# Kernel optimization log

Measured on AMD Instinct MI355X. Metric: run time of the kernel, lower is better.

## Reference

```python
import jax, jax.numpy as jnp
import numpy as np

N, M, D, K = 32768, 1024, 512, 4096  # frames, motion_dim, latent_dim, codebook size
COMMITMENT_COST = 0.25
BN_EPS = 1e-5


def setup_inputs() -> dict:
    key = jax.random.key(0)
    ks = jax.random.split(key, 4)
    return {
        "x": jax.random.normal(ks[0], (N, M), dtype=jnp.float32),
        "enc_w": jax.random.normal(ks[1], (D, M), dtype=jnp.float32) * (1.0 / np.sqrt(M)),
        "enc_b": jnp.zeros((D,), jnp.float32),
        "bn_gamma": jnp.ones((D,), jnp.float32),
        "bn_beta": jnp.zeros((D,), jnp.float32),
        "bn_mean": jnp.zeros((D,), jnp.float32),
        "bn_var": jnp.ones((D,), jnp.float32),
        # nn.Embedding init: uniform(-1/K, 1/K)
        "codebook": jax.random.uniform(ks[2], (K, D), dtype=jnp.float32, minval=-1.0 / K, maxval=1.0 / K),
        "dec_w": jax.random.normal(ks[3], (M, D), dtype=jnp.float32) * (1.0 / np.sqrt(D)),
        "dec_b": jnp.zeros((M,), jnp.float32),
    }


def reference(x, enc_w, enc_b, bn_gamma, bn_beta, bn_mean, bn_var, codebook, dec_w, dec_b):
    # Encoder linear: [N, M] -> [N, D]
    z = x @ enc_w.T + enc_b
    # BatchNorm1d (inference mode, running stats)
    z = (z - bn_mean) * jax.lax.rsqrt(bn_var + BN_EPS) * bn_gamma + bn_beta

    # VQ (VQ_Payam_EMA, eval): squared L2 distances via ||z||^2 + ||e||^2 - 2 z e^T
    # distances: [N, K]
    distances = (
        jnp.sum(z * z, axis=1, keepdims=True)
        + jnp.sum(codebook * codebook, axis=1)
        - 2.0 * (z @ codebook.T)
    )
    idx = jnp.argmin(distances, axis=1)                    # [N]
    encodings = jax.nn.one_hot(idx, K, dtype=z.dtype)      # [N, K] one-hot scatter
    quantized = codebook[idx]                              # gather == encodings @ codebook

    # commitment loss (EMA variant: only e_latent_loss, quantized detached)
    e_latent_loss = jnp.mean((jax.lax.stop_gradient(quantized) - z) ** 2)
    loss = COMMITMENT_COST * e_latent_loss

    # straight-through estimator
    quantized_st = z + jax.lax.stop_gradient(quantized - z)

    avg_probs = jnp.mean(encodings, axis=0)                # [K]
    perplexity = jnp.exp(-jnp.sum(avg_probs * jnp.log(avg_probs + 1e-10)))

    # Decoder linear: [N, D] -> [N, M]
    out = quantized_st @ dec_w.T + dec_b
    return out, loss, perplexity, encodings
```

## Files before the change

kernel.cpp:

```cpp
#include <hip/hip_runtime.h>
#include <math.h>
#include <float.h>

#define N_FR 32768
#define M_DIM 1024
#define D_DIM 512
#define K_CB 4096

static const long long OUT_ELEMS = (long long)N_FR * M_DIM;
static const long long LOSS_OFF  = OUT_ELEMS;
static const long long ENC_OFF   = OUT_ELEMS + 2;
static const long long Z_OFF     = ENC_OFF + 2;
static const long long DC_OFF    = Z_OFF  + (long long)N_FR * D_DIM;
static const long long XH_OFF    = DC_OFF + (long long)K_CB * M_DIM;
static const long long XL_OFF    = XH_OFF + (long long)N_FR * M_DIM / 2;
static const long long WH_OFF    = XL_OFF + (long long)N_FR * M_DIM / 2;
static const long long WL_OFF    = WH_OFF + (long long)D_DIM * M_DIM / 2;
static const long long CH_OFF    = WL_OFF + (long long)D_DIM * M_DIM / 2;
static const long long CL_OFF    = CH_OFF + (long long)K_CB * D_DIM / 2;
static const long long ZH_OFF    = CL_OFF + (long long)K_CB * D_DIM / 2;
static const long long ZL_OFF    = ZH_OFF + (long long)N_FR * D_DIM / 2;
static const long long PV_OFF    = ZL_OFF + (long long)N_FR * D_DIM / 2;
static const long long PI_OFF    = PV_OFF + 4LL * N_FR;
static const long long DWH_OFF   = PI_OFF + 4LL * N_FR;
static const long long DWL_OFF   = DWH_OFF + (long long)M_DIM * D_DIM / 2;
static const long long SN_OFF    = DWL_OFF + (long long)M_DIM * D_DIM / 2;
static const long long LP_OFF    = SN_OFF + (long long)N_FR;

typedef __attribute__((ext_vector_type(8))) short bf16x8;
typedef __attribute__((ext_vector_type(8))) unsigned short u16x8;
typedef __attribute__((ext_vector_type(4))) float f32x4;

__device__ __forceinline__ unsigned short f2bf(float f) {
    unsigned u = __float_as_uint(f);
    return (unsigned short)((u + 0x7fffu + ((u >> 16) & 1u)) >> 16);
}
__device__ __forceinline__ float bf2f(unsigned short h) {
    return __uint_as_float(((unsigned)h) << 16);
}
__device__ __forceinline__ void gl_lds16(const unsigned short* g, unsigned short* l) {
    __builtin_amdgcn_global_load_lds(
        (const __attribute__((address_space(1))) unsigned int*)g,
        (__attribute__((address_space(3))) unsigned int*)l,
        16, 0, 0);
}

__device__ __forceinline__ void conv_body(const float* in, unsigned short* hi,
                                          unsigned short* lo, int C, int KC, int w)
{
    int lane = threadIdx.x & 63;
    int bn = w / KC, ck = w % KC;
    int r = bn * 16 + (lane & 15);
    int c = ck * 32 + (lane >> 4) * 8;
    const float4* p = (const float4*)&in[(size_t)r * C + c];
    float4 v0 = p[0], v1 = p[1];
    float f[8] = {v0.x, v0.y, v0.z, v0.w, v1.x, v1.y, v1.z, v1.w};
    u16x8 hv, lv;
    #pragma unroll
    for (int j = 0; j < 8; ++j) {
        unsigned short h = f2bf(f[j]);
        hv[j] = h;
        lv[j] = f2bf(f[j] - bf2f(h));
    }
    size_t o = (size_t)w * 512 + lane * 8;
    *(u16x8*)&hi[o] = hv;
    *(u16x8*)&lo[o] = lv;
}

__global__ __launch_bounds__(256)
void conv_all(const float* __restrict__ x,  const float* __restrict__ ew,
              const float* __restrict__ cb, const float* __restrict__ dw,
              unsigned short* __restrict__ xh,  unsigned short* __restrict__ xl,
              unsigned short* __restrict__ wh,  unsigned short* __restrict__ wl,
              unsigned short* __restrict__ ch,  unsigned short* __restrict__ cl,
              unsigned short* __restrict__ dwh, unsigned short* __restrict__ dwl)
{
    int b = blockIdx.x;
    const float* in; unsigned short* hi; unsigned short* lo; int C; int w0;
    if (b < 16384)      { in = x;  hi = xh;  lo = xl;  C = 1024; w0 = b; }
    else if (b < 16640) { in = ew; hi = wh;  lo = wl;  C = 1024; w0 = b - 16384; }
    else if (b < 17664) { in = cb; hi = ch;  lo = cl;  C = 512;  w0 = b - 16640; }
    else                { in = dw; hi = dwh; lo = dwl; C = 512;  w0 = b - 17664; }
    int KC = C / 32;
    conv_body(in, hi, lo, C, KC, w0 * 4 + (threadIdx.x >> 6));
}

__global__ __launch_bounds__(256)
void conv_split(const float* __restrict__ in, unsigned short* __restrict__ hi,
                unsigned short* __restrict__ lo, int C, int KC)
{
    conv_body(in, hi, lo, C, KC, blockIdx.x * 4 + (threadIdx.x >> 6));
}

template<int EPI>
__global__ __launch_bounds__(256)
void gemm_pack(const unsigned short* __restrict__ ah_, const unsigned short* __restrict__ al_,
               const unsigned short* __restrict__ bh_, const unsigned short* __restrict__ bl_,
               const float* __restrict__ bias, const float* __restrict__ gamma,
               const float* __restrict__ beta, const float* __restrict__ mean,
               const float* __restrict__ var, float* __restrict__ C,
               int nbi, int nkb, int NJ)
{
    __shared__ unsigned short lds[16384];
    const int tid = threadIdx.x, wid = tid >> 6, lane = tid & 63;
    const int wr = wid >> 1, wc = wid & 1;
    const int bi = blockIdx.x % nbi, bj = blockIdx.x / nbi;

    f32x4 acc[4][4];
    #pragma unroll
    for (int i = 0; i < 4; ++i)
        #pragma unroll
        for (int j = 0; j < 4; ++j) acc[i][j] = (f32x4){0.f, 0.f, 0.f, 0.f};

    for (int ks = 0; ks < nkb; ++ks) {
        __syncthreads();
        #pragma unroll
        for (int q = 0; q < 8; ++q) {
            int id = wid * 8 + q;
            int arr = id >> 3, rb = id & 7;
            const unsigned short* base = arr == 0 ? ah_ : arr == 1 ? al_ : arr == 2 ? bh_ : bl_;
            size_t b = (size_t)((arr < 2 ? bi : bj) * 8 + rb) * nkb + ks;
            gl_lds16(base + b * 512 + lane * 8, lds + id * 512);
        }
        __syncthreads();
        bf16x8 ah[4], al[4], bh[4], bl[4];
        #pragma unroll
        for (int i = 0; i < 4; ++i) {
            ah[i] = *(const bf16x8*)(lds + (4 * wr + i) * 512 + lane * 8);
            al[i] = *(const bf16x8*)(lds + 4096 + (4 * wr + i) * 512 + lane * 8);
        }
        #pragma unroll
        for (int j = 0; j < 4; ++j) {
            bh[j] = *(const bf16x8*)(lds + 8192  + (4 * wc + j) * 512 + lane * 8);
            bl[j] = *(const bf16x8*)(lds + 12288 + (4 * wc + j) * 512 + lane * 8);
        }
        #pragma unroll
        for (int i = 0; i < 4; ++i)
            #pragma unroll
            for (int j = 0; j < 4; ++j) {
                acc[i][j] = __builtin_amdgcn_mfma_f32_16x16x32_bf16(ah[i], bh[j], acc[i][j], 0, 0, 0);
                acc[i][j] = __builtin_amdgcn_mfma_f32_16x16x32_bf16(ah[i], bl[j], acc[i][j], 0, 0, 0);
                acc[i][j] = __builtin_amdgcn_mfma_f32_16x16x32_bf16(al[i], bh[j], acc[i][j], 0, 0, 0);
            }
    }
    #pragma unroll
    for (int j = 0; j < 4; ++j) {
        int col = bj * 128 + wc * 64 + j * 16 + (lane & 15);
        float bvv = bias[col];
        float g = 0.f, bt = 0.f, mn = 0.f, rs = 0.f;
        if (EPI == 0) {
            g  = gamma[col];
            bt = beta[col];
            mn = mean[col];
            rs = (float)(1.0 / sqrt((double)var[col] + 1e-5));
        }
        #pragma unroll
        for (int i = 0; i < 4; ++i)
            #pragma unroll
            for (int r = 0; r < 4; ++r) {
                int row = bi * 128 + wr * 64 + i * 16 + (lane >> 4) * 4 + r;
                float v = acc[i][j][r] + bvv;
                if (EPI == 0) v = (v - mn) * rs * g + bt;
                C[(size_t)row * NJ + col] = v;
            }
    }
}

__global__ __launch_bounds__(256, 2)
void argmin_mfma(const unsigned short* __restrict__ zh, const unsigned short* __restrict__ zl,
                 const unsigned short* __restrict__ ch,
                 const float* __restrict__ se,
                 float* __restrict__ pval, int* __restrict__ pidx)
{
    __shared__ unsigned short lds[32768];
    __shared__ float sv[128][2];
    __shared__ int   si[128][2];
    const int tid = threadIdx.x, wid = tid >> 6, lane = tid & 63;
    const int wr = wid >> 1, wc = wid & 1;
    const int row0 = (int)(blockIdx.x >> 2) * 128;
    const int grp  = (int)(blockIdx.x & 3);

    auto stage = [&](int t, int bufsel) {
        int cc = t >> 4, ks = t & 15;
        int code0 = grp * 1024 + cc * 256;
        unsigned short* dst = lds + bufsel * 16384;
        #pragma unroll
        for (int q = 0; q < 8; ++q) {
            int id = wid * 8 + q;
            const unsigned short* src;
            if (id < 16) {
                int a = id >> 3, rb = id & 7;
                src = (a ? zl : zh) + ((size_t)((row0 >> 4) + rb) * 16 + ks) * 512 + lane * 8;
            } else {
                int cb2 = id - 16;
                src = ch + ((size_t)((code0 >> 4) + cb2) * 16 + ks) * 512 + lane * 8;
            }
            gl_lds16(src, dst + id * 512);
        }
    };

    float bv[16];
    int   bi[16];
    #pragma unroll
    for (int s = 0; s < 16; ++s) { bv[s] = FLT_MAX; bi[s] = 0x7fffffff; }

    f32x4 acc[4][8];
    #pragma unroll
    for (int i = 0; i < 4; ++i)
        #pragma unroll
        for (int j = 0; j < 8; ++j) acc[i][j] = (f32x4){0.f, 0.f, 0.f, 0.f};

    stage(0, 0);
    __syncthreads();

    for (int t = 0; t < 64; ++t) {
        int cur = t & 1;
        if (t < 63) stage(t + 1, cur ^ 1);
        const unsigned short* L = lds + cur * 16384;
        bf16x8 ah[4], al[4];
        #pragma unroll
        for (int i = 0; i < 4; ++i) {
            ah[i] = *(const bf16x8*)(L + (wr * 4 + i) * 512 + lane * 8);
            al[i] = *(const bf16x8*)(L + 4096 + (wr * 4 + i) * 512 + lane * 8);
        }
        #pragma unroll
        for (int j = 0; j < 8; ++j) {
            bf16x8 bhj = *(const bf16x8*)(L + 8192 + (wc * 8 + j) * 512 + lane * 8);
            #pragma unroll
            for (int i = 0; i < 4; ++i) {
                acc[i][j] = __builtin_amdgcn_mfma_f32_16x16x32_bf16(ah[i], bhj, acc[i][j], 0, 0, 0);
                acc[i][j] = __builtin_amdgcn_mfma_f32_16x16x32_bf16(al[i], bhj, acc[i][j], 0, 0, 0);
            }
        }
        if ((t & 15) == 15) {
            int code0 = grp * 1024 + (t >> 4) * 256;
            #pragma unroll
            for (int j = 0; j < 8; ++j) {
                int code = code0 + wc * 128 + j * 16 + (lane & 15);
                float sev = se[code];
                #pragma unroll
                for (int i = 0; i < 4; ++i)
                    #pragma unroll
                    for (int r = 0; r < 4; ++r) {
                        float key = sev - 2.0f * acc[i][j][r];
                        int s = i * 4 + r;
                        if (key < bv[s]) { bv[s] = key; bi[s] = code; }
                        acc[i][j][r] = 0.f;
                    }
            }
        }
        __syncthreads();
    }

    #pragma unroll
    for (int s = 0; s < 16; ++s) {
        #pragma unroll
        for (int off = 1; off < 16; off <<= 1) {
            float ov = __shfl_xor(bv[s], off);
            int   oi = __shfl_xor(bi[s], off);
            if (ov < bv[s] || (ov == bv[s] && oi < bi[s])) { bv[s] = ov; bi[s] = oi; }
        }
    }
    if ((lane & 15) == 0) {
        #pragma unroll
        for (int i = 0; i < 4; ++i)
            #pragma unroll
            for (int r = 0; r < 4; ++r) {
                int row = wr * 64 + i * 16 + (lane >> 4) * 4 + r;
                sv[row][wc] = bv[i * 4 + r];
                si[row][wc] = bi[i * 4 + r];
            }
    }
    __syncthreads();
    if (tid < 128) {
        float v0 = sv[tid][0], v1 = sv[tid][1];
        int   i0 = si[tid][0], i1 = si[tid][1];
        float bvv = v0; int bii = i0;
        if (v1 < v0 || (v1 == v0 && i1 < i0)) { bvv = v1; bii = i1; }
        pval[(size_t)grp * N_FR + row0 + tid] = bvv;
        pidx[(size_t)grp * N_FR + row0 + tid] = bii;
    }
}

__global__ __launch_bounds__(256)
void merge_k(const float* __restrict__ pval, const int* __restrict__ pidx,
             const float* __restrict__ sn,
             int* __restrict__ fidx, int* __restrict__ counts,
             float* __restrict__ lpart)
{
    __shared__ float ls[4];
    int tid = threadIdx.x;
    int n = blockIdx.x * 256 + tid;
    float best = pval[n];
    int   bi   = pidx[n];
    #pragma unroll
    for (int c = 1; c < 4; ++c) {
        float v = pval[(long long)c * N_FR + n];
        int   i = pidx[(long long)c * N_FR + n];
        if (v < best) { best = v; bi = i; }
    }
    fidx[n] = bi;
    atomicAdd(&counts[bi], 1);
    float rl = sn[n] + best;
    #pragma unroll
    for (int off = 32; off; off >>= 1) rl += __shfl_xor(rl, off);
    if ((tid & 63) == 0) ls[tid >> 6] = rl;
    __syncthreads();
    if (tid == 0) lpart[blockIdx.x] = ls[0] + ls[1] + ls[2] + ls[3];
}

__global__ __launch_bounds__(256)
void rownorm_k(const float* __restrict__ A, float* __restrict__ sn)
{
    int row  = blockIdx.x * 4 + (threadIdx.x >> 6);
    int lane = threadIdx.x & 63;
    const float4* p = (const float4*)(A + (long long)row * D_DIM + lane * 8);
    float4 a = p[0], b = p[1];
    float s = a.x*a.x + a.y*a.y + a.z*a.z + a.w*a.w
            + b.x*b.x + b.y*b.y + b.z*b.z + b.w*b.w;
    #pragma unroll
    for (int off = 32; off; off >>= 1) s += __shfl_xor(s, off);
    if (lane == 0) sn[row] = s;
}

__global__ __launch_bounds__(256)
void gather_k(const float* __restrict__ DC, const int* __restrict__ fidx,
              float* __restrict__ outp)
{
    int n = blockIdx.x;
    int id = fidx[n];
    float4 v = ((const float4*)(DC + (long long)id * M_DIM))[threadIdx.x];
    ((float4*)(outp + (long long)n * M_DIM))[threadIdx.x] = v;
}

__global__ __launch_bounds__(256)
void enc_write(const int* __restrict__ fidx, float* __restrict__ enc)
{
    int n    = blockIdx.x * 4 + (threadIdx.x >> 6);
    int lane = threadIdx.x & 63;
    int idx  = fidx[n];
    float4* row = (float4*)(enc + (size_t)n * K_CB);
    #pragma unroll
    for (int c = 0; c < 16; ++c) {
        int p = c * 64 + lane;
        int b4 = p * 4;
        float4 v;
        v.x = (idx == b4 + 0) ? 1.0f : 0.0f;
        v.y = (idx == b4 + 1) ? 1.0f : 0.0f;
        v.z = (idx == b4 + 2) ? 1.0f : 0.0f;
        v.w = (idx == b4 + 3) ? 1.0f : 0.0f;
        row[p] = v;
    }
}

__global__ __launch_bounds__(256)
void fin_k(const int* __restrict__ counts, const float* __restrict__ lpart,
           float* __restrict__ scal)
{
    __shared__ double sh[4], lh[4];
    int tid = threadIdx.x;
    double s = 0.0;
    for (int k = tid; k < K_CB; k += 256) {
        double p = (double)counts[k] / (double)N_FR;
        s += p * log(p + 1e-10);
    }
    double l = (tid < 128) ? (double)lpart[tid] : 0.0;
    #pragma unroll
    for (int off = 32; off; off >>= 1) {
        s += __shfl_xor(s, off);
        l += __shfl_xor(l, off);
    }
    if ((tid & 63) == 0) { sh[tid >> 6] = s; lh[tid >> 6] = l; }
    __syncthreads();
    if (tid == 0) {
        double tot = sh[0] + sh[1] + sh[2] + sh[3];
        double L   = lh[0] + lh[1] + lh[2] + lh[3];
        scal[0] = (float)(0.25 * L / ((double)N_FR * (double)D_DIM));
        scal[1] = (float)exp(-tot);
    }
}

extern "C" void kernel_launch(void* const* d_in, const int* in_sizes, int n_in,
                              void* d_out, int out_size, void* d_ws, size_t ws_size,
                              hipStream_t stream)
{
    (void)in_sizes; (void)n_in; (void)out_size; (void)ws_size;
    const float* x        = (const float*)d_in[0];
    const float* enc_w    = (const float*)d_in[1];
    const float* enc_b    = (const float*)d_in[2];
    const float* bn_gamma = (const float*)d_in[3];
    const float* bn_beta  = (const float*)d_in[4];
    const float* bn_mean  = (const float*)d_in[5];
    const float* bn_var   = (const float*)d_in[6];
    const float* cb       = (const float*)d_in[7];
    const float* dec_w    = (const float*)d_in[8];
    const float* dec_b    = (const float*)d_in[9];

    float* outp = (float*)d_out;
    float* z    = outp + Z_OFF;
    float* dc   = outp + DC_OFF;
    unsigned short* xh  = (unsigned short*)(outp + XH_OFF);
    unsigned short* xl  = (unsigned short*)(outp + XL_OFF);
    unsigned short* whp = (unsigned short*)(outp + WH_OFF);
    unsigned short* wlp = (unsigned short*)(outp + WL_OFF);
    unsigned short* chp = (unsigned short*)(outp + CH_OFF);
    unsigned short* clp = (unsigned short*)(outp + CL_OFF);
    unsigned short* zhp = (unsigned short*)(outp + ZH_OFF);
    unsigned short* zlp = (unsigned short*)(outp + ZL_OFF);
    float* pval = outp + PV_OFF;
    int*   pidx = (int*)(outp + PI_OFF);
    unsigned short* dwh = (unsigned short*)(outp + DWH_OFF);
    unsigned short* dwl = (unsigned short*)(outp + DWL_OFF);
    float* sn    = outp + SN_OFF;
    float* lpart = outp + LP_OFF;

    char*   wsb    = (char*)d_ws;
    int*    fidx   = (int*)wsb;
    int*    counts = (int*)(wsb + 131072);
    float*  se     = (float*)(wsb + 147456);

    hipMemsetAsync(counts, 0, 16384, stream);

    conv_all<<<dim3(17920), 256, 0, stream>>>(x, enc_w, cb, dec_w,
        xh, xl, whp, wlp, chp, clp, dwh, dwl);
    rownorm_k<<<dim3(K_CB / 4), 256, 0, stream>>>(cb, se);

    gemm_pack<0><<<dim3(1024), 256, 0, stream>>>(xh, xl, whp, wlp,
        enc_b, bn_gamma, bn_beta, bn_mean, bn_var, z, 256, 32, D_DIM);
    conv_split<<<dim3(8192), 256, 0, stream>>>(z, zhp, zlp, D_DIM, D_DIM / 32);
    rownorm_k<<<dim3(N_FR / 4), 256, 0, stream>>>(z, sn);

    gemm_pack<1><<<dim3(256), 256, 0, stream>>>(chp, clp, dwh, dwl,
        dec_b, nullptr, nullptr, nullptr, nullptr, dc, 32, 16, M_DIM);

    argmin_mfma<<<dim3(1024), 256, 0, stream>>>(zhp, zlp, chp, se, pval, pidx);
    merge_k<<<dim3(N_FR / 256), 256, 0, stream>>>(pval, pidx, sn, fidx, counts, lpart);

    gather_k<<<dim3(N_FR), 256, 0, stream>>>(dc, fidx, outp);
    fin_k<<<dim3(1), 256, 0, stream>>>(counts, lpart, outp + LOSS_OFF);

    enc_write<<<dim3(N_FR / 4), 256, 0, stream>>>(fidx, outp + ENC_OFF);
}
```

Before: 662.2 us.

## Drop low-order bf16 split terms for weights, codebook and z; double-buffer GEMMs

Removes the low-part bf16 residual for the encoder weights, the codebook and z. The encoder and decoder GEMMs therefore do two MFMA passes instead of three, and the argmin distance GEMM does one instead of two. The GEMM kernel gains double-buffered LDS staging. The z conversion is fused with the row-norm computation into one kernel that writes partial sums, and merge_k adds those up. This cuts MFMA work and memory traffic, but lowers precision in the distance computation, which can flip argmin results for near-tied codebook entries.

```diff
diff --git a/kernel.cpp b/kernel.cpp
--- a/kernel.cpp
+++ b/kernel.cpp
@@ -10,22 +10,19 @@
 static const long long OUT_ELEMS = (long long)N_FR * M_DIM;
 static const long long LOSS_OFF  = OUT_ELEMS;
 static const long long ENC_OFF   = OUT_ELEMS + 2;
-static const long long Z_OFF     = ENC_OFF + 2;
-static const long long DC_OFF    = Z_OFF  + (long long)N_FR * D_DIM;
-static const long long XH_OFF    = DC_OFF + (long long)K_CB * M_DIM;
-static const long long XL_OFF    = XH_OFF + (long long)N_FR * M_DIM / 2;
-static const long long WH_OFF    = XL_OFF + (long long)N_FR * M_DIM / 2;
-static const long long WL_OFF    = WH_OFF + (long long)D_DIM * M_DIM / 2;
-static const long long CH_OFF    = WL_OFF + (long long)D_DIM * M_DIM / 2;
-static const long long CL_OFF    = CH_OFF + (long long)K_CB * D_DIM / 2;
-static const long long ZH_OFF    = CL_OFF + (long long)K_CB * D_DIM / 2;
-static const long long ZL_OFF    = ZH_OFF + (long long)N_FR * D_DIM / 2;
-static const long long PV_OFF    = ZL_OFF + (long long)N_FR * D_DIM / 2;
-static const long long PI_OFF    = PV_OFF + 4LL * N_FR;
-static const long long DWH_OFF   = PI_OFF + 4LL * N_FR;
-static const long long DWL_OFF   = DWH_OFF + (long long)M_DIM * D_DIM / 2;
-static const long long SN_OFF    = DWL_OFF + (long long)M_DIM * D_DIM / 2;
-static const long long LP_OFF    = SN_OFF + (long long)N_FR;
+static const long long Z_OFF   = ENC_OFF + 2;
+static const long long DC_OFF  = Z_OFF  + (long long)N_FR * D_DIM;
+static const long long XH_OFF  = DC_OFF + (long long)K_CB * M_DIM;
+static const long long XL_OFF  = XH_OFF + (long long)N_FR * M_DIM / 2;
+static const long long WH_OFF  = XL_OFF + (long long)N_FR * M_DIM / 2;
+static const long long CH_OFF  = WH_OFF + (long long)D_DIM * M_DIM / 2;
+static const long long ZH_OFF  = CH_OFF + (long long)K_CB * D_DIM / 2;
+static const long long PV_OFF  = ZH_OFF + (long long)N_FR * D_DIM / 2;
+static const long long PI_OFF  = PV_OFF + 4LL * N_FR;
+static const long long DWH_OFF = PI_OFF + 4LL * N_FR;
+static const long long DWL_OFF = DWH_OFF + (long long)M_DIM * D_DIM / 2;
+static const long long SNP_OFF = DWL_OFF + (long long)M_DIM * D_DIM / 2;
+static const long long LP_OFF  = SNP_OFF + 16LL * N_FR;
 
 typedef __attribute__((ext_vector_type(8))) short bf16x8;
 typedef __attribute__((ext_vector_type(8))) unsigned short u16x8;
@@ -64,91 +61,120 @@
     }
     size_t o = (size_t)w * 512 + lane * 8;
     *(u16x8*)&hi[o] = hv;
-    *(u16x8*)&lo[o] = lv;
+    if (lo) *(u16x8*)&lo[o] = lv;
 }
 
 __global__ __launch_bounds__(256)
 void conv_all(const float* __restrict__ x,  const float* __restrict__ ew,
               const float* __restrict__ cb, const float* __restrict__ dw,
               unsigned short* __restrict__ xh,  unsigned short* __restrict__ xl,
-              unsigned short* __restrict__ wh,  unsigned short* __restrict__ wl,
-              unsigned short* __restrict__ ch,  unsigned short* __restrict__ cl,
+              unsigned short* __restrict__ wh,
+              unsigned short* __restrict__ ch,
               unsigned short* __restrict__ dwh, unsigned short* __restrict__ dwl)
 {
     int b = blockIdx.x;
     const float* in; unsigned short* hi; unsigned short* lo; int C; int w0;
-    if (b < 16384)      { in = x;  hi = xh;  lo = xl;  C = 1024; w0 = b; }
-    else if (b < 16640) { in = ew; hi = wh;  lo = wl;  C = 1024; w0 = b - 16384; }
-    else if (b < 17664) { in = cb; hi = ch;  lo = cl;  C = 512;  w0 = b - 16640; }
-    else                { in = dw; hi = dwh; lo = dwl; C = 512;  w0 = b - 17664; }
+    if (b < 16384)      { in = x;  hi = xh;  lo = xl;      C = 1024; w0 = b; }
+    else if (b < 16640) { in = ew; hi = wh;  lo = nullptr; C = 1024; w0 = b - 16384; }
+    else if (b < 17664) { in = cb; hi = ch;  lo = nullptr; C = 512;  w0 = b - 16640; }
+    else                { in = dw; hi = dwh; lo = dwl;     C = 512;  w0 = b - 17664; }
     int KC = C / 32;
     conv_body(in, hi, lo, C, KC, w0 * 4 + (threadIdx.x >> 6));
 }
 
 __global__ __launch_bounds__(256)
-void conv_split(const float* __restrict__ in, unsigned short* __restrict__ hi,
-                unsigned short* __restrict__ lo, int C, int KC)
-{
-    conv_body(in, hi, lo, C, KC, blockIdx.x * 4 + (threadIdx.x >> 6));
-}
-
-template<int EPI>
-__global__ __launch_bounds__(256)
-void gemm_pack(const unsigned short* __restrict__ ah_, const unsigned short* __restrict__ al_,
-               const unsigned short* __restrict__ bh_, const unsigned short* __restrict__ bl_,
-               const float* __restrict__ bias, const float* __restrict__ gamma,
-               const float* __restrict__ beta, const float* __restrict__ mean,
-               const float* __restrict__ var, float* __restrict__ C,
-               int nbi, int nkb, int NJ)
-{
-    __shared__ unsigned short lds[16384];
+void conv_z(const float* __restrict__ z, unsigned short* __restrict__ zh,
+            float* __restrict__ snp)
+{
+    int w = blockIdx.x * 4 + (threadIdx.x >> 6);
+    int lane = threadIdx.x & 63;
+    int bn = w >> 4, ck = w & 15;
+    int r = bn * 16 + (lane & 15);
+    int c = ck * 32 + (lane >> 4) * 8;
+    const float4* p = (const float4*)&z[(size_t)r * D_DIM + c];
+    float4 v0 = p[0], v1 = p[1];
+    float f[8] = {v0.x, v0.y, v0.z, v0.w, v1.x, v1.y, v1.z, v1.w};
+    u16x8 hv;
+    float s = 0.f;
+    #pragma unroll
+    for (int j = 0; j < 8; ++j) {
+        hv[j] = f2bf(f[j]);
+        s = fmaf(f[j], f[j], s);
+    }
+    *(u16x8*)&zh[(size_t)w * 512 + lane * 8] = hv;
+    s += __shfl_xor(s, 16);
+    s += __shfl_xor(s, 32);
+    if ((lane >> 4) == 0) snp[(size_t)ck * N_FR + r] = s;
+}
+
+template<int MODE>
+__global__ __launch_bounds__(256, 2)
+void gemm2(const unsigned short* __restrict__ s0_, const unsigned short* __restrict__ s1_,
+           const unsigned short* __restrict__ s2_,
+           const float* __restrict__ bias, const float* __restrict__ gamma,
+           const float* __restrict__ beta, const float* __restrict__ mean,
+           const float* __restrict__ var, float* __restrict__ C,
+           int nbi, int nkb, int NJ)
+{
+    __shared__ unsigned short lds[24576];
     const int tid = threadIdx.x, wid = tid >> 6, lane = tid & 63;
     const int wr = wid >> 1, wc = wid & 1;
     const int bi = blockIdx.x % nbi, bj = blockIdx.x / nbi;
 
+    auto stage = [&](int ks, int bufsel) {
+        unsigned short* dst = lds + bufsel * 12288;
+        #pragma unroll
+        for (int q = 0; q < 6; ++q) {
+            int id = wid * 6 + q;
+            int arr = id >> 3, rb = id & 7;
+            const unsigned short* base = arr == 0 ? s0_ : arr == 1 ? s1_ : s2_;
+            int bsel = (arr == 0) ? bi : (arr == 1 ? (MODE == 0 ? bi : bj) : bj);
+            size_t b = (size_t)(bsel * 8 + rb) * nkb + ks;
+            gl_lds16(base + b * 512 + lane * 8, dst + id * 512);
+        }
+    };
+
     f32x4 acc[4][4];
     #pragma unroll
     for (int i = 0; i < 4; ++i)
         #pragma unroll
         for (int j = 0; j < 4; ++j) acc[i][j] = (f32x4){0.f, 0.f, 0.f, 0.f};
 
+    stage(0, 0);
+    __syncthreads();
+
     for (int ks = 0; ks < nkb; ++ks) {
-        __syncthreads();
-        #pragma unroll
-        for (int q = 0; q < 8; ++q) {
-            int id = wid * 8 + q;
-            int arr = id >> 3, rb = id & 7;
-            const unsigned short* base = arr == 0 ? ah_ : arr == 1 ? al_ : arr == 2 ? bh_ : bl_;
-            size_t b = (size_t)((arr < 2 ? bi : bj) * 8 + rb) * nkb + ks;
-            gl_lds16(base + b * 512 + lane * 8, lds + id * 512);
-        }
-        __syncthreads();
-        bf16x8 ah[4], al[4], bh[4], bl[4];
+        int cur = ks & 1;
+        if (ks + 1 < nkb) stage(ks + 1, cur ^ 1);
+        const unsigned short* L = lds + cur * 12288;
+        bf16x8 r0[4], r1[4], r2[4];
         #pragma unroll
         for (int i = 0; i < 4; ++i) {
-            ah[i] = *(const bf16x8*)(lds + (4 * wr + i) * 512 + lane * 8);
-            al[i] = *(const bf16x8*)(lds + 4096 + (4 * wr + i) * 512 + lane * 8);
-        }
-        #pragma unroll
-        for (int j = 0; j < 4; ++j) {
-            bh[j] = *(const bf16x8*)(lds + 8192  + (4 * wc + j) * 512 + lane * 8);
-            bl[j] = *(const bf16x8*)(lds + 12288 + (4 * wc + j) * 512 + lane * 8);
+            r0[i] = *(const bf16x8*)(L + (wr * 4 + i) * 512 + lane * 8);
+            r1[i] = *(const bf16x8*)(L + 4096 + ((MODE == 0 ? wr : wc) * 4 + i) * 512 + lane * 8);
+            r2[i] = *(const bf16x8*)(L + 8192 + (wc * 4 + i) * 512 + lane * 8);
         }
         #pragma unroll
         for (int i = 0; i < 4; ++i)
             #pragma unroll
             for (int j = 0; j < 4; ++j) {
-                acc[i][j] = __builtin_amdgcn_mfma_f32_16x16x32_bf16(ah[i], bh[j], acc[i][j], 0, 0, 0);
-                acc[i][j] = __builtin_amdgcn_mfma_f32_16x16x32_bf16(ah[i], bl[j], acc[i][j], 0, 0, 0);
-                acc[i][j] = __builtin_amdgcn_mfma_f32_16x16x32_bf16(al[i], bh[j], acc[i][j], 0, 0, 0);
+                if (MODE == 0) {
+                    acc[i][j] = __builtin_amdgcn_mfma_f32_16x16x32_bf16(r0[i], r2[j], acc[i][j], 0, 0, 0);
+                    acc[i][j] = __builtin_amdgcn_mfma_f32_16x16x32_bf16(r1[i], r2[j], acc[i][j], 0, 0, 0);
+                } else {
+                    acc[i][j] = __builtin_amdgcn_mfma_f32_16x16x32_bf16(r0[i], r1[j], acc[i][j], 0, 0, 0);
+                    acc[i][j] = __builtin_amdgcn_mfma_f32_16x16x32_bf16(r0[i], r2[j], acc[i][j], 0, 0, 0);
+                }
             }
-    }
+        __syncthreads();
+    }
+
     #pragma unroll
     for (int j = 0; j < 4; ++j) {
         int col = bj * 128 + wc * 64 + j * 16 + (lane & 15);
         float bvv = bias[col];
         float g = 0.f, bt = 0.f, mn = 0.f, rs = 0.f;
-        if (EPI == 0) {
+        if (MODE == 0) {
             g  = gamma[col];
             bt = beta[col];
             mn = mean[col];
@@ -160,19 +186,18 @@
             for (int r = 0; r < 4; ++r) {
                 int row = bi * 128 + wr * 64 + i * 16 + (lane >> 4) * 4 + r;
                 float v = acc[i][j][r] + bvv;
-                if (EPI == 0) v = (v - mn) * rs * g + bt;
+                if (MODE == 0) v = (v - mn) * rs * g + bt;
                 C[(size_t)row * NJ + col] = v;
             }
     }
 }
 
 __global__ __launch_bounds__(256, 2)
-void argmin_mfma(const unsigned short* __restrict__ zh, const unsigned short* __restrict__ zl,
-                 const unsigned short* __restrict__ ch,
+void argmin_mfma(const unsigned short* __restrict__ zh, const unsigned short* __restrict__ ch,
                  const float* __restrict__ se,
                  float* __restrict__ pval, int* __restrict__ pidx)
 {
-    __shared__ unsigned short lds[32768];
+    __shared__ unsigned short lds[24576];
     __shared__ float sv[128][2];
     __shared__ int   si[128][2];
     const int tid = threadIdx.x, wid = tid >> 6, lane = tid & 63;
@@ -183,16 +208,15 @@
     auto stage = [&](int t, int bufsel) {
         int cc = t >> 4, ks = t & 15;
         int code0 = grp * 1024 + cc * 256;
-        unsigned short* dst = lds + bufsel * 16384;
-        #pragma unroll
-        for (int q = 0; q < 8; ++q) {
-            int id = wid * 8 + q;
+        unsigned short* dst = lds + bufsel * 12288;
+        #pragma unroll
+        for (int q = 0; q < 6; ++q) {
+            int id = wid * 6 + q;
             const unsigned short* src;
-            if (id < 16) {
-                int a = id >> 3, rb = id & 7;
-                src = (a ? zl : zh) + ((size_t)((row0 >> 4) + rb) * 16 + ks) * 512 + lane * 8;
+            if (id < 8) {
+                src = zh + ((size_t)((row0 >> 4) + id) * 16 + ks) * 512 + lane * 8;
             } else {
-                int cb2 = id - 16;
+                int cb2 = id - 8;
                 src = ch + ((size_t)((code0 >> 4) + cb2) * 16 + ks) * 512 + lane * 8;
             }
             gl_lds16(src, dst + id * 512);
@@ -216,21 +240,17 @@
     for (int t = 0; t < 64; ++t) {
         int cur = t & 1;
         if (t < 63) stage(t + 1, cur ^ 1);
-        const unsigned short* L = lds + cur * 16384;
-        bf16x8 ah[4], al[4];
-        #pragma unroll
-        for (int i = 0; i < 4; ++i) {
+        const unsigned short* L = lds + cur * 12288;
+        bf16x8 ah[4];
+        #pragma unroll
+        for (int i = 0; i < 4; ++i)
             ah[i] = *(const bf16x8*)(L + (wr * 4 + i) * 512 + lane * 8);
-            al[i] = *(const bf16x8*)(L + 4096 + (wr * 4 + i) * 512 + lane * 8);
-        }
         #pragma unroll
         for (int j = 0; j < 8; ++j) {
-            bf16x8 bhj = *(const bf16x8*)(L + 8192 + (wc * 8 + j) * 512 + lane * 8);
+            bf16x8 bhj = *(const bf16x8*)(L + 4096 + (wc * 8 + j) * 512 + lane * 8);
             #pragma unroll
-            for (int i = 0; i < 4; ++i) {
+            for (int i = 0; i < 4; ++i)
                 acc[i][j] = __builtin_amdgcn_mfma_f32_16x16x32_bf16(ah[i], bhj, acc[i][j], 0, 0, 0);
-                acc[i][j] = __builtin_amdgcn_mfma_f32_16x16x32_bf16(al[i], bhj, acc[i][j], 0, 0, 0);
-            }
         }
         if ((t & 15) == 15) {
             int code0 = grp * 1024 + (t >> 4) * 256;
@@ -284,7 +304,7 @@
 
 __global__ __launch_bounds__(256)
 void merge_k(const float* __restrict__ pval, const int* __restrict__ pidx,
-             const float* __restrict__ sn,
+             const float* __restrict__ snp,
              int* __restrict__ fidx, int* __restrict__ counts,
              float* __restrict__ lpart)
 {
@@ -301,7 +321,10 @@
     }
     fidx[n] = bi;
     atomicAdd(&counts[bi], 1);
-    float rl = sn[n] + best;
+    float sn = 0.f;
+    #pragma unroll
+    for (int c = 0; c < 16; ++c) sn += snp[(long long)c * N_FR + n];
+    float rl = sn + best;
     #pragma unroll
     for (int off = 32; off; off >>= 1) rl += __shfl_xor(rl, off);
     if ((tid & 63) == 0) ls[tid >> 6] = rl;
@@ -402,16 +425,13 @@
     unsigned short* xh  = (unsigned short*)(outp + XH_OFF);
     unsigned short* xl  = (unsigned short*)(outp + XL_OFF);
     unsigned short* whp = (unsigned short*)(outp + WH_OFF);
-    unsigned short* wlp = (unsigned short*)(outp + WL_OFF);
     unsigned short* chp = (unsigned short*)(outp + CH_OFF);
-    unsigned short* clp = (unsigned short*)(outp + CL_OFF);
     unsigned short* zhp = (unsigned short*)(outp + ZH_OFF);
-    unsigned short* zlp = (unsigned short*)(outp + ZL_OFF);
     float* pval = outp + PV_OFF;
     int*   pidx = (int*)(outp + PI_OFF);
     unsigned short* dwh = (unsigned short*)(outp + DWH_OFF);
     unsigned short* dwl = (unsigned short*)(outp + DWL_OFF);
-    float* sn    = outp + SN_OFF;
+    float* snp   = outp + SNP_OFF;
     float* lpart = outp + LP_OFF;
 
     char*   wsb    = (char*)d_ws;
@@ -422,19 +442,18 @@
     hipMemsetAsync(counts, 0, 16384, stream);
 
     conv_all<<<dim3(17920), 256, 0, stream>>>(x, enc_w, cb, dec_w,
-        xh, xl, whp, wlp, chp, clp, dwh, dwl);
+        xh, xl, whp, chp, dwh, dwl);
     rownorm_k<<<dim3(K_CB / 4), 256, 0, stream>>>(cb, se);
 
-    gemm_pack<0><<<dim3(1024), 256, 0, stream>>>(xh, xl, whp, wlp,
+    gemm2<0><<<dim3(1024), 256, 0, stream>>>(xh, xl, whp,
         enc_b, bn_gamma, bn_beta, bn_mean, bn_var, z, 256, 32, D_DIM);
-    conv_split<<<dim3(8192), 256, 0, stream>>>(z, zhp, zlp, D_DIM, D_DIM / 32);
-    rownorm_k<<<dim3(N_FR / 4), 256, 0, stream>>>(z, sn);
-
-    gemm_pack<1><<<dim3(256), 256, 0, stream>>>(chp, clp, dwh, dwl,
+    conv_z<<<dim3(8192), 256, 0, stream>>>(z, zhp, snp);
+
+    gemm2<1><<<dim3(256), 256, 0, stream>>>(chp, dwh, dwl,
         dec_b, nullptr, nullptr, nullptr, nullptr, dc, 32, 16, M_DIM);
 
-    argmin_mfma<<<dim3(1024), 256, 0, stream>>>(zhp, zlp, chp, se, pval, pidx);
-    merge_k<<<dim3(N_FR / 256), 256, 0, stream>>>(pval, pidx, sn, fidx, counts, lpart);
+    argmin_mfma<<<dim3(1024), 256, 0, stream>>>(zhp, chp, se, pval, pidx);
+    merge_k<<<dim3(N_FR / 256), 256, 0, stream>>>(pval, pidx, snp, fidx, counts, lpart);
 
     gather_k<<<dim3(N_FR), 256, 0, stream>>>(dc, fidx, outp);
     fin_k<<<dim3(1), 256, 0, stream>>>(counts, lpart, outp + LOSS_OFF);
```

New measurement: 726.7 us. 9.7% more time.
